# Optimization experiments

Measured on AMD Instinct MI355X. Metric: run time of the kernel, lower is better.

The kernel has to match this reference:

```python
import jax, jax.numpy as jnp
import numpy as np

WINDOW_SIZE = 256
NEG_INF = jnp.finfo(jnp.float32).min


def setup_inputs() -> dict:
    key = jax.random.key(0)
    kq, kk, kv = jax.random.split(key, 3)
    B, H, S, D = 1, 8, 4096, 128
    q = jax.random.normal(kq, (B, H, S, D), dtype=jnp.float32)
    k = jax.random.normal(kk, (B, H, S, D), dtype=jnp.float32)
    v = jax.random.normal(kv, (B, H, S, D), dtype=jnp.float32)
    return {"q": q, "k": k, "v": v}


def _local_mask(seq_len: int) -> jnp.ndarray:
    idx = jnp.arange(seq_len)
    qi = idx[:, None]
    ki = idx[None, :]
    # causal AND within trailing window of WINDOW_SIZE keys
    return (ki <= qi) & (ki >= qi - WINDOW_SIZE + 1)  # [S, S] bool


def reference(q, k, v):
    B, H, S, D = q.shape
    scale = 1.0 / np.sqrt(D).astype(np.float32)
    mask = _local_mask(S)  # [S, S]
    scores = jnp.einsum('bhsd,bhtd->bhst', q, k) * scale  # [B,H,S,S]
    scores = jnp.where(mask[None, None, :, :], scores, NEG_INF)
    attn = jax.nn.softmax(scores.astype(jnp.float32), axis=-1).astype(q.dtype)
    out = jnp.einsum('bhst,bhtd->bhsd', attn, v)
    return out
```

## Files before the change

kernel.cpp:

```cpp
#include <hip/hip_runtime.h>


typedef __bf16 bf16v8 __attribute__((ext_vector_type(8)));
typedef __bf16 bf16x2 __attribute__((ext_vector_type(2)));
typedef float  f32x4  __attribute__((ext_vector_type(4)));

constexpr int QB = 64, DH = 128, WIN = 256, KT = 64;
constexpr int NTILE = 5, NSUB = 20;
constexpr float SCALE = 0.08838834764831844f;

constexpr int PSTR = 328;
constexpr int VT0  = 43008;
constexpr int VT1  = VT0 + 16384;
constexpr int SMEM_BYTES = VT1 + 16384;

union bfu8 { bf16v8 v; bf16x2 p[4]; };

__device__ __forceinline__ void cvt_hilo8(const float4& a, const float4& b,
                                          bf16v8& hi, bf16v8& lo) {
  float x[8] = {a.x, a.y, a.z, a.w, b.x, b.y, b.z, b.w};
  bfu8 H, L;
#pragma unroll
  for (int j = 0; j < 4; ++j) {
    float x0 = x[2 * j], x1 = x[2 * j + 1];
    __bf16 h0 = (__bf16)x0, h1 = (__bf16)x1;
    H.p[j] = bf16x2{h0, h1};
    L.p[j] = bf16x2{(__bf16)(x0 - (float)h0), (__bf16)(x1 - (float)h1)};
  }
  hi = H.v; lo = L.v;
}
__device__ __forceinline__ bf16v8 cvt8(const float4& a, const float4& b) {
  float x[8] = {a.x, a.y, a.z, a.w, b.x, b.y, b.z, b.w};
  bfu8 H;
#pragma unroll
  for (int j = 0; j < 4; ++j)
    H.p[j] = bf16x2{(__bf16)x[2 * j], (__bf16)x[2 * j + 1]};
  return H.v;
}
__device__ __forceinline__ unsigned short bfbits(float x) {
  union { __bf16 b; unsigned short u; } c; c.b = (__bf16)x; return c.u;
}
#define MFMA(A, B, C) __builtin_amdgcn_mfma_f32_16x16x32_bf16((A), (B), (C), 0, 0, 0)

__global__ __launch_bounds__(256, 2)
void lwa5(const float* __restrict__ qg, const float* __restrict__ kg,
          const float* __restrict__ vg, float* __restrict__ og, int S) {
  __shared__ __align__(16) char smem[SMEM_BYTES];

  const int bid = blockIdx.x;
  const int h   = bid & 7;
  const int q0  = (bid >> 3) * QB;
  const int tid = threadIdx.x;
  const int wv  = tid >> 6;
  const int lane = tid & 63;
  const int lg  = lane >> 4;
  const int lm  = lane & 15;

  const float* qgb = qg + (size_t)h * S * DH;
  const float* kgb = kg + (size_t)h * S * DH;
  const float* vgb = vg + (size_t)h * S * DH;

  bf16v8 qhi[4], qlo[4];
  {
    const float* qrow = qgb + (size_t)(q0 + 16 * wv + lm) * DH;
#pragma unroll
    for (int kc = 0; kc < 4; ++kc) {
      const int d0 = 32 * kc + 8 * lg;
      float4 a = *(const float4*)(qrow + d0);
      float4 b = *(const float4*)(qrow + d0 + 4);
      a.x *= SCALE; a.y *= SCALE; a.z *= SCALE; a.w *= SCALE;
      b.x *= SCALE; b.y *= SCALE; b.z *= SCALE; b.w *= SCALE;
      cvt_hilo8(a, b, qhi[kc], qlo[kc]);
    }
  }

  f32x4 acc[NSUB];
#pragma unroll
  for (int t = 0; t < NSUB; ++t) acc[t] = (f32x4){0.f, 0.f, 0.f, 0.f};

  float4 kbuf[2][8];
  auto kload = [&](int s, int buf) {
    const int key0 = q0 - WIN + 16 * s;
    if (key0 < 0) return;
    const float* kr = kgb + (size_t)(key0 + lm) * DH;
#pragma unroll
    for (int kc = 0; kc < 4; ++kc) {
      kbuf[buf][2 * kc]     = *(const float4*)(kr + 32 * kc + 8 * lg);
      kbuf[buf][2 * kc + 1] = *(const float4*)(kr + 32 * kc + 8 * lg + 4);
    }
  };
  kload(0, 0);
#pragma unroll
  for (int s = 0; s < NSUB; ++s) {
    if (s + 1 < NSUB) kload(s + 1, (s + 1) & 1);
    if (q0 - WIN + 16 * s >= 0) {
      f32x4 c = acc[s];
#pragma unroll
      for (int kc = 0; kc < 4; ++kc) {
        bf16v8 kh, kl;
        cvt_hilo8(kbuf[s & 1][2 * kc], kbuf[s & 1][2 * kc + 1], kh, kl);
        c = MFMA(qhi[kc], kh, c);
        c = MFMA(qlo[kc], kh, c);
        c = MFMA(qhi[kc], kl, c);
      }
      acc[s] = c;
    }
  }

  const int srow = tid >> 4;
  const int sd0  = (tid & 15) * 8;
  auto vload = [&](int kt0, float4 r[8]) {
#pragma unroll
    for (int i = 0; i < 4; ++i) {
      const float* p = vgb + (size_t)(kt0 + srow + 16 * i) * DH + sd0;
      r[2 * i]     = *(const float4*)(p);
      r[2 * i + 1] = *(const float4*)(p + 4);
    }
  };
  auto vwrite = [&](char* dst, const float4 r[8]) {
#pragma unroll
    for (int i = 0; i < 4; ++i) {
      const int key = srow + 16 * i;
      float x[8] = {r[2*i].x, r[2*i].y, r[2*i].z, r[2*i].w,
                    r[2*i+1].x, r[2*i+1].y, r[2*i+1].z, r[2*i+1].w};
#pragma unroll
      for (int j = 0; j < 8; ++j) {
        const int d = sd0 + j;
        const int swz = ((d & 7) ^ ((d >> 3) & 7)) << 4;
        *(unsigned short*)(dst + d * 128 + ((key * 2) ^ swz)) = bfbits(x[j]);
      }
    }
  };

  const int kt0_0 = q0 - WIN, kt0_1 = q0 - WIN + KT;
  float4 vr0[8], vr1[8];
  if (kt0_0 >= 0) vload(kt0_0, vr0);
  if (kt0_1 >= 0) vload(kt0_1, vr1);

  float rl[4];
#pragma unroll
  for (int r = 0; r < 4; ++r) {
    const int qi = q0 + 16 * wv + 4 * lg + r;
    float m = -3.0e38f;
#pragma unroll
    for (int ts = 0; ts < NSUB; ++ts) {
      const int ki = q0 - WIN + 16 * ts + lm;
      const bool ok = (ki >= 0) && (ki <= qi) && (ki > qi - WIN);
      float s = ok ? acc[ts][r] : -3.0e38f;
      acc[ts][r] = s;
      m = fmaxf(m, s);
    }
#pragma unroll
    for (int msk = 1; msk < 16; msk <<= 1) m = fmaxf(m, __shfl_xor(m, msk));
    float l = 0.f;
#pragma unroll
    for (int ts = 0; ts < NSUB; ++ts) {
      float p = __expf(acc[ts][r] - m);
      acc[ts][r] = p;
      l += p;
    }
#pragma unroll
    for (int msk = 1; msk < 16; msk <<= 1) l += __shfl_xor(l, msk);
    rl[r] = 1.f / l;
  }

#pragma unroll
  for (int ts = 0; ts < NSUB; ++ts)
#pragma unroll
    for (int r = 0; r < 4; ++r) {
      const int row = 16 * wv + 4 * lg + r;
      const int col = 16 * ts + lm;
      *(unsigned short*)(smem + row * (PSTR * 2) + col * 2) = bfbits(acc[ts][r]);
    }

  if (kt0_0 >= 0) vwrite(smem + VT0, vr0);
  if (kt0_1 >= 0) vwrite(smem + VT1, vr1);
  __syncthreads();

  f32x4 o[8];
#pragma unroll
  for (int n = 0; n < 8; ++n) o[n] = (f32x4){0.f, 0.f, 0.f, 0.f};

#pragma unroll
  for (int t = 0; t < NTILE; ++t) {
    const int kt0 = q0 - WIN + t * KT;
    const int tp  = t + 2;
    const int ktp = q0 - WIN + tp * KT;
    float4 pre[8];
    if (tp < NTILE && ktp >= 0) vload(ktp, pre);
    if (kt0 >= 0) {
      const char* vbuf = smem + ((t & 1) ? VT1 : VT0);
#pragma unroll
      for (int kc = 0; kc < 2; ++kc) {
        const int colb = (16 * wv + lm) * (PSTR * 2) + 128 * t + 64 * kc + 16 * lg;
        bf16v8 pf = *(const bf16v8*)(smem + colb);
#pragma unroll
        for (int n = 0; n < 8; ++n) {
          const int d = 16 * n + lm;
          const int swz = ((d & 7) ^ ((d >> 3) & 7)) << 4;
          bf16v8 vf = *(const bf16v8*)(vbuf + d * 128 + ((64 * kc + 16 * lg) ^ swz));
          o[n] = MFMA(pf, vf, o[n]);
        }
      }
    }
    if (tp < NTILE) {
      __syncthreads();
      if (ktp >= 0) vwrite(smem + ((t & 1) ? VT1 : VT0), pre);
      __syncthreads();
    }
  }

  float* orow = og + ((size_t)(h * S + q0 + 16 * wv)) * DH;
#pragma unroll
  for (int n = 0; n < 8; ++n)
#pragma unroll
    for (int r = 0; r < 4; ++r)
      orow[(4 * lg + r) * DH + 16 * n + lm] = o[n][r] * rl[r];
}

extern "C" void kernel_launch(void* const* d_in, const int* in_sizes, int n_in,
                              void* d_out, int out_size, void* d_ws, size_t ws_size,
                              hipStream_t stream) {
  const float* q = (const float*)d_in[0];
  const float* k = (const float*)d_in[1];
  const float* v = (const float*)d_in[2];
  float* out = (float*)d_out;
  const int H = 8, D = 128;
  const int S = in_sizes[0] / (H * D);
  const int nblk = (S / QB) * H;
  lwa5<<<dim3(nblk), 256, 0, stream>>>(q, k, v, out, S);
}
```

Baseline: 129.5 us.

## Halve query block and split keys and head dim across wave pairs

Reduces the query block to 32 rows and splits each block's four waves into two row groups by two key halves. Row max and row sum are combined across halves through shared memory, and each half then computes half of the head dimension in the PV product. V tiles are no longer staged in LDS with swizzle; each lane gathers V directly from global memory with strided scalar loads and converts them to bf16. The aim is more blocks, higher occupancy (launch bounds 4) and less LDS traffic and sync. The costs are more redundant K and V global reads per query and uncoalesced V loads.

```diff
diff --git a/kernel.cpp b/kernel.cpp
--- a/kernel.cpp
+++ b/kernel.cpp
@@ -5,14 +5,15 @@
 typedef __bf16 bf16x2 __attribute__((ext_vector_type(2)));
 typedef float  f32x4  __attribute__((ext_vector_type(4)));
 
-constexpr int QB = 64, DH = 128, WIN = 256, KT = 64;
-constexpr int NTILE = 5, NSUB = 20;
+constexpr int QB = 32, DH = 128, WIN = 256;
+constexpr int HSUB = 9;
 constexpr float SCALE = 0.08838834764831844f;
 
-constexpr int PSTR = 328;
-constexpr int VT0  = 43008;
-constexpr int VT1  = VT0 + 16384;
-constexpr int SMEM_BYTES = VT1 + 16384;
+constexpr int PSTR  = 296;
+constexpr int P_BYTES = QB * PSTR * 2;
+constexpr int MB_OFF  = P_BYTES;
+constexpr int LB_OFF  = MB_OFF + 64 * 4;
+constexpr int SMEM_BYTES = LB_OFF + 64 * 4;
 
 union bfu8 { bf16v8 v; bf16x2 p[4]; };
 
@@ -29,21 +30,13 @@
   }
   hi = H.v; lo = L.v;
 }
-__device__ __forceinline__ bf16v8 cvt8(const float4& a, const float4& b) {
-  float x[8] = {a.x, a.y, a.z, a.w, b.x, b.y, b.z, b.w};
-  bfu8 H;
-#pragma unroll
-  for (int j = 0; j < 4; ++j)
-    H.p[j] = bf16x2{(__bf16)x[2 * j], (__bf16)x[2 * j + 1]};
-  return H.v;
-}
 __device__ __forceinline__ unsigned short bfbits(float x) {
   union { __bf16 b; unsigned short u; } c; c.b = (__bf16)x; return c.u;
 }
 #define MFMA(A, B, C) __builtin_amdgcn_mfma_f32_16x16x32_bf16((A), (B), (C), 0, 0, 0)
 
-__global__ __launch_bounds__(256, 2)
-void lwa5(const float* __restrict__ qg, const float* __restrict__ kg,
+__global__ __launch_bounds__(256, 4)
+void lwa6(const float* __restrict__ qg, const float* __restrict__ kg,
           const float* __restrict__ vg, float* __restrict__ og, int S) {
   __shared__ __align__(16) char smem[SMEM_BYTES];
 
@@ -55,6 +48,9 @@
   const int lane = tid & 63;
   const int lg  = lane >> 4;
   const int lm  = lane & 15;
+  const int rg  = wv & 1;
+  const int hf  = wv >> 1;
+  const int ts0 = HSUB * hf;
 
   const float* qgb = qg + (size_t)h * S * DH;
   const float* kgb = kg + (size_t)h * S * DH;
@@ -62,160 +58,126 @@
 
   bf16v8 qhi[4], qlo[4];
   {
-    const float* qrow = qgb + (size_t)(q0 + 16 * wv + lm) * DH;
+    const float* qrow = qgb + (size_t)(q0 + 16 * rg + lm) * DH;
 #pragma unroll
     for (int kc = 0; kc < 4; ++kc) {
-      const int d0 = 32 * kc + 8 * lg;
-      float4 a = *(const float4*)(qrow + d0);
-      float4 b = *(const float4*)(qrow + d0 + 4);
+      float4 a = *(const float4*)(qrow + 32 * kc + 8 * lg);
+      float4 b = *(const float4*)(qrow + 32 * kc + 8 * lg + 4);
       a.x *= SCALE; a.y *= SCALE; a.z *= SCALE; a.w *= SCALE;
       b.x *= SCALE; b.y *= SCALE; b.z *= SCALE; b.w *= SCALE;
       cvt_hilo8(a, b, qhi[kc], qlo[kc]);
     }
   }
 
-  f32x4 acc[NSUB];
+  f32x4 acc[HSUB];
 #pragma unroll
-  for (int t = 0; t < NSUB; ++t) acc[t] = (f32x4){0.f, 0.f, 0.f, 0.f};
+  for (int s = 0; s < HSUB; ++s) acc[s] = (f32x4){0.f, 0.f, 0.f, 0.f};
 
-  float4 kbuf[2][8];
-  auto kload = [&](int s, int buf) {
-    const int key0 = q0 - WIN + 16 * s;
-    if (key0 < 0) return;
+#pragma unroll
+  for (int s = 0; s < HSUB; ++s) {
+    const int key0 = q0 - WIN + 16 * (ts0 + s);
+    if (key0 < 0) continue;
     const float* kr = kgb + (size_t)(key0 + lm) * DH;
+    float4 ka[4], kb_[4];
 #pragma unroll
     for (int kc = 0; kc < 4; ++kc) {
-      kbuf[buf][2 * kc]     = *(const float4*)(kr + 32 * kc + 8 * lg);
-      kbuf[buf][2 * kc + 1] = *(const float4*)(kr + 32 * kc + 8 * lg + 4);
+      ka[kc]  = *(const float4*)(kr + 32 * kc + 8 * lg);
+      kb_[kc] = *(const float4*)(kr + 32 * kc + 8 * lg + 4);
     }
-  };
-  kload(0, 0);
+    f32x4 c = acc[s];
 #pragma unroll
-  for (int s = 0; s < NSUB; ++s) {
-    if (s + 1 < NSUB) kload(s + 1, (s + 1) & 1);
-    if (q0 - WIN + 16 * s >= 0) {
-      f32x4 c = acc[s];
-#pragma unroll
-      for (int kc = 0; kc < 4; ++kc) {
-        bf16v8 kh, kl;
-        cvt_hilo8(kbuf[s & 1][2 * kc], kbuf[s & 1][2 * kc + 1], kh, kl);
-        c = MFMA(qhi[kc], kh, c);
-        c = MFMA(qlo[kc], kh, c);
-        c = MFMA(qhi[kc], kl, c);
-      }
-      acc[s] = c;
+    for (int kc = 0; kc < 4; ++kc) {
+      bf16v8 kh, kl;
+      cvt_hilo8(ka[kc], kb_[kc], kh, kl);
+      c = MFMA(qhi[kc], kh, c);
+      c = MFMA(qlo[kc], kh, c);
+      c = MFMA(qhi[kc], kl, c);
     }
+    acc[s] = c;
   }
 
-  const int srow = tid >> 4;
-  const int sd0  = (tid & 15) * 8;
-  auto vload = [&](int kt0, float4 r[8]) {
-#pragma unroll
-    for (int i = 0; i < 4; ++i) {
-      const float* p = vgb + (size_t)(kt0 + srow + 16 * i) * DH + sd0;
-      r[2 * i]     = *(const float4*)(p);
-      r[2 * i + 1] = *(const float4*)(p + 4);
-    }
-  };
-  auto vwrite = [&](char* dst, const float4 r[8]) {
-#pragma unroll
-    for (int i = 0; i < 4; ++i) {
-      const int key = srow + 16 * i;
-      float x[8] = {r[2*i].x, r[2*i].y, r[2*i].z, r[2*i].w,
-                    r[2*i+1].x, r[2*i+1].y, r[2*i+1].z, r[2*i+1].w};
-#pragma unroll
-      for (int j = 0; j < 8; ++j) {
-        const int d = sd0 + j;
-        const int swz = ((d & 7) ^ ((d >> 3) & 7)) << 4;
-        *(unsigned short*)(dst + d * 128 + ((key * 2) ^ swz)) = bfbits(x[j]);
-      }
-    }
-  };
+  float* mbuf = (float*)(smem + MB_OFF);
+  float* lbuf = (float*)(smem + LB_OFF);
 
-  const int kt0_0 = q0 - WIN, kt0_1 = q0 - WIN + KT;
-  float4 vr0[8], vr1[8];
-  if (kt0_0 >= 0) vload(kt0_0, vr0);
-  if (kt0_1 >= 0) vload(kt0_1, vr1);
-
-  float rl[4];
+  float mrow[4], rl[4];
 #pragma unroll
   for (int r = 0; r < 4; ++r) {
-    const int qi = q0 + 16 * wv + 4 * lg + r;
+    const int qi = q0 + 16 * rg + 4 * lg + r;
     float m = -3.0e38f;
 #pragma unroll
-    for (int ts = 0; ts < NSUB; ++ts) {
-      const int ki = q0 - WIN + 16 * ts + lm;
+    for (int s = 0; s < HSUB; ++s) {
+      const int ki = q0 - WIN + 16 * (ts0 + s) + lm;
       const bool ok = (ki >= 0) && (ki <= qi) && (ki > qi - WIN);
-      float s = ok ? acc[ts][r] : -3.0e38f;
-      acc[ts][r] = s;
-      m = fmaxf(m, s);
+      float v = ok ? acc[s][r] : -3.0e38f;
+      acc[s][r] = v;
+      m = fmaxf(m, v);
     }
 #pragma unroll
     for (int msk = 1; msk < 16; msk <<= 1) m = fmaxf(m, __shfl_xor(m, msk));
+    mrow[r] = m;
+    if (lm == 0) mbuf[hf * 32 + 16 * rg + 4 * lg + r] = m;
+  }
+  __syncthreads();
+#pragma unroll
+  for (int r = 0; r < 4; ++r)
+    mrow[r] = fmaxf(mrow[r], mbuf[(1 - hf) * 32 + 16 * rg + 4 * lg + r]);
+
+#pragma unroll
+  for (int r = 0; r < 4; ++r) {
     float l = 0.f;
 #pragma unroll
-    for (int ts = 0; ts < NSUB; ++ts) {
-      float p = __expf(acc[ts][r] - m);
-      acc[ts][r] = p;
+    for (int s = 0; s < HSUB; ++s) {
+      float p = __expf(acc[s][r] - mrow[r]);
+      acc[s][r] = p;
       l += p;
     }
 #pragma unroll
     for (int msk = 1; msk < 16; msk <<= 1) l += __shfl_xor(l, msk);
-    rl[r] = 1.f / l;
+    if (lm == 0) lbuf[hf * 32 + 16 * rg + 4 * lg + r] = l;
+    rl[r] = l;
+    const int row = 16 * rg + 4 * lg + r;
+#pragma unroll
+    for (int s = 0; s < HSUB; ++s) {
+      const int col = 16 * (ts0 + s) + lm;
+      *(unsigned short*)(smem + row * (PSTR * 2) + col * 2) = bfbits(acc[s][r]);
+    }
   }
+  __syncthreads();
+#pragma unroll
+  for (int r = 0; r < 4; ++r)
+    rl[r] = 1.f / (rl[r] + lbuf[(1 - hf) * 32 + 16 * rg + 4 * lg + r]);
+
+  f32x4 o[4];
+#pragma unroll
+  for (int n = 0; n < 4; ++n) o[n] = (f32x4){0.f, 0.f, 0.f, 0.f};
 
 #pragma unroll
-  for (int ts = 0; ts < NSUB; ++ts)
+  for (int kc = 0; kc < 9; ++kc) {
+    const int keyb = q0 - WIN + 32 * kc;
+    if (keyb < 0) continue;
+    const bf16v8 pf = *(const bf16v8*)(smem + (16 * rg + lm) * (PSTR * 2) +
+                                       (32 * kc + 8 * lg) * 2);
 #pragma unroll
-    for (int r = 0; r < 4; ++r) {
-      const int row = 16 * wv + 4 * lg + r;
-      const int col = 16 * ts + lm;
-      *(unsigned short*)(smem + row * (PSTR * 2) + col * 2) = bfbits(acc[ts][r]);
-    }
-
-  if (kt0_0 >= 0) vwrite(smem + VT0, vr0);
-  if (kt0_1 >= 0) vwrite(smem + VT1, vr1);
-  __syncthreads();
-
-  f32x4 o[8];
+    for (int n = 0; n < 4; ++n) {
+      const int d = 64 * hf + 16 * n + lm;
+      const float* vp = vgb + (size_t)(keyb + 8 * lg) * DH + d;
+      float x[8];
 #pragma unroll
-  for (int n = 0; n < 8; ++n) o[n] = (f32x4){0.f, 0.f, 0.f, 0.f};
-
+      for (int j = 0; j < 8; ++j) x[j] = vp[(size_t)j * DH];
+      bfu8 V_;
 #pragma unroll
-  for (int t = 0; t < NTILE; ++t) {
-    const int kt0 = q0 - WIN + t * KT;
-    const int tp  = t + 2;
-    const int ktp = q0 - WIN + tp * KT;
-    float4 pre[8];
-    if (tp < NTILE && ktp >= 0) vload(ktp, pre);
-    if (kt0 >= 0) {
-      const char* vbuf = smem + ((t & 1) ? VT1 : VT0);
-#pragma unroll
-      for (int kc = 0; kc < 2; ++kc) {
-        const int colb = (16 * wv + lm) * (PSTR * 2) + 128 * t + 64 * kc + 16 * lg;
-        bf16v8 pf = *(const bf16v8*)(smem + colb);
-#pragma unroll
-        for (int n = 0; n < 8; ++n) {
-          const int d = 16 * n + lm;
-          const int swz = ((d & 7) ^ ((d >> 3) & 7)) << 4;
-          bf16v8 vf = *(const bf16v8*)(vbuf + d * 128 + ((64 * kc + 16 * lg) ^ swz));
-          o[n] = MFMA(pf, vf, o[n]);
-        }
-      }
-    }
-    if (tp < NTILE) {
-      __syncthreads();
-      if (ktp >= 0) vwrite(smem + ((t & 1) ? VT1 : VT0), pre);
-      __syncthreads();
+      for (int j = 0; j < 4; ++j)
+        V_.p[j] = bf16x2{(__bf16)x[2 * j], (__bf16)x[2 * j + 1]};
+      o[n] = MFMA(pf, V_.v, o[n]);
     }
   }
 
-  float* orow = og + ((size_t)(h * S + q0 + 16 * wv)) * DH;
+  float* ob = og + (size_t)(h * S + q0 + 16 * rg) * DH;
 #pragma unroll
-  for (int n = 0; n < 8; ++n)
+  for (int n = 0; n < 4; ++n)
 #pragma unroll
     for (int r = 0; r < 4; ++r)
-      orow[(4 * lg + r) * DH + 16 * n + lm] = o[n][r] * rl[r];
+      ob[(4 * lg + r) * DH + 64 * hf + 16 * n + lm] = o[n][r] * rl[r];
 }
 
 extern "C" void kernel_launch(void* const* d_in, const int* in_sizes, int n_in,
@@ -228,5 +190,5 @@
   const int H = 8, D = 128;
   const int S = in_sizes[0] / (H * D);
   const int nblk = (S / QB) * H;
-  lwa5<<<dim3(nblk), 256, 0, stream>>>(q, k, v, out, S);
+  lwa6<<<dim3(nblk), 256, 0, stream>>>(q, k, v, out, S);
 }
```

Result: no change. 128.9 us (-0.5%).
